# Optimization experiments

Hardware: AMD Instinct MI355X
Metric: run time of the kernel (lower is better)

The kernel has to match this reference:

```python
import jax, jax.numpy as jnp
import numpy as np

NUM_HEADS = 12
DIM = 768


def _ste_sign(x):
    # forward: sign with sign(0) = +1; backward: pass-through on |x| <= 1
    s = jnp.where(x >= 0, 1.0, -1.0).astype(x.dtype)
    base = jnp.clip(x, -1.0, 1.0)
    return base + jax.lax.stop_gradient(s - base)


def _quantize_qk(x):
    # s = mean(|x|) over last two dims (differentiable), times STE sign
    s = jnp.mean(jnp.abs(x), axis=(-2, -1), keepdims=True)
    return s * _ste_sign(x)


def _round_ste(z):
    return z + jax.lax.stop_gradient(jnp.round(z) - z)


def _quantize_p(x):
    qmax = 255.0
    s = 1.0 / qmax
    q = jnp.clip(_round_ste(x / s), 0.0, qmax)
    return s * q


def _quantize_v(x):
    # SymQuantizer fwd: per-column (dim=-2) absmax, detached; 8-bit symmetric
    m = jax.lax.stop_gradient(jnp.max(jnp.abs(x), axis=-2, keepdims=True))
    s = 127.0 / (m + 1e-6)
    qz = jnp.round(x * s) / (s + 1e-6)
    # backward STE: pass-through where -2 < x < 2 (clip_val = [-2, 2])
    base = jnp.clip(x, -2.0, 2.0)
    return base + jax.lax.stop_gradient(qz - base)


def _attention(x, w_qkv, w_proj, b_proj):
    B, C, H, W = x.shape
    N = H * W
    nh = NUM_HEADS
    hd = C // nh
    scale = hd ** (-0.5)
    xf = x.reshape(B, C, N).transpose(0, 2, 1)          # [B, N, C]
    qkv = xf @ w_qkv.T                                   # [B, N, 3C]
    qkv = qkv.reshape(B, N, 3, nh, hd).transpose(2, 0, 3, 1, 4)  # [3, B, h, N, d]
    q, k, v = qkv[0], qkv[1], qkv[2]
    q = _quantize_qk(q)
    k = _quantize_qk(k)
    attn = jnp.einsum('bhnd,bhmd->bhnm', q, k) * scale   # [B, h, N, N]
    attn = jax.nn.softmax(attn, axis=-1)
    attn = _quantize_p(attn)
    v = _quantize_v(v)
    out = jnp.einsum('bhnm,bhmd->bhnd', attn, v)         # [B, h, N, d]
    out = out.transpose(0, 2, 1, 3).reshape(B, N, C)
    out = out @ w_proj.T + b_proj                        # [B, N, C]
    return out.transpose(0, 2, 1).reshape(B, C, H, W)


def setup_inputs() -> dict:
    key = jax.random.key(0)
    k1, k2, k3, k4 = jax.random.split(key, 4)
    B, C, H, W = 16, DIM, 24, 24
    x = jax.random.normal(k1, (B, C, H, W), dtype=jnp.float32)
    w_qkv = jax.random.normal(k2, (3 * C, C), dtype=jnp.float32) * 0.02
    w_proj = jax.random.normal(k3, (C, C), dtype=jnp.float32) * 0.02
    b_proj = jax.random.normal(k4, (C,), dtype=jnp.float32) * 0.02
    return {"x": x, "w_qkv": w_qkv, "w_proj": w_proj, "b_proj": b_proj}


def reference(x, w_qkv, w_proj, b_proj):
    return _attention(x, w_qkv, w_proj, b_proj)
```

## Files before the change

### kernel.cpp

```cpp
#include <hip/hip_runtime.h>
#include <hip/hip_bf16.h>

#define B_   16
#define NH   12
#define NTOK 576
#define HD   64
#define CH   768
#define NELEM (B_*NH*NTOK*HD)
#define VT8SZ (NTOK*HD)
#define FIXCAP 16384
#define VPAD 176

typedef short v8s __attribute__((ext_vector_type(8)));
typedef short v4s __attribute__((ext_vector_type(4)));
typedef float v4f __attribute__((ext_vector_type(4)));
typedef int   v4i __attribute__((ext_vector_type(4)));

static __device__ __forceinline__ void split4(const float* f, v4s& hi, v4s& lo)
{
    #pragma unroll
    for (int i = 0; i < 4; ++i) {
        __hip_bfloat16 h = __float2bfloat16(f[i]);
        float hf = __bfloat162float(h);
        __hip_bfloat16 l = __float2bfloat16(f[i] - hf);
        hi[i] = __builtin_bit_cast(short, h);
        lo[i] = __builtin_bit_cast(short, l);
    }
}

__global__ __launch_bounds__(256) void qkv_mfma(const float* __restrict__ x,
    const float* __restrict__ w, float* __restrict__ q, float* __restrict__ k,
    float* __restrict__ v, int* __restrict__ fixn_g)
{
    if (blockIdx.x == 0 && threadIdx.x == 0) *fixn_g = 0;

    __shared__ short Ah[64*40], Al[64*40];
    __shared__ short Bh[256*40], Bl[256*40];
    const int tid = threadIdx.x;
    int g = blockIdx.x;
    g = (g & 7) * 162 + (g >> 3);
    const int b  = g / 81;
    const int rr = g % 81;
    const int jb = rr / 9;
    const int mb = rr % 9;
    const int n0 = mb * 64;
    const int j0 = jb * 256;
    const int lane = tid & 63, wv = tid >> 6;

    const int cq  = tid & 7;
    const int rw0 = tid >> 3;

    const float* xb  = x + (size_t)b * CH * NTOK + n0;
    const float* wbp = w + (size_t)j0 * CH;

    float areg[2][4];
    float breg[8][4];

    #pragma unroll
    for (int s = 0; s < 2; ++s) {
        const int nl = rw0 + 32*s;
        #pragma unroll
        for (int i = 0; i < 4; ++i)
            areg[s][i] = xb[(size_t)(cq*4 + i) * NTOK + nl];
    }
    #pragma unroll
    for (int s = 0; s < 8; ++s) {
        const int jl = rw0 + 32*s;
        const float4 t = *(const float4*)(wbp + (size_t)jl * CH + cq*4);
        breg[s][0]=t.x; breg[s][1]=t.y; breg[s][2]=t.z; breg[s][3]=t.w;
    }

    v4f acc[4][4];
    #pragma unroll
    for (int a = 0; a < 4; ++a)
        #pragma unroll
        for (int c = 0; c < 4; ++c) acc[a][c] = (v4f){0.f,0.f,0.f,0.f};

    for (int it = 0; it < 24; ++it) {
        __syncthreads();
        #pragma unroll
        for (int s = 0; s < 2; ++s) {
            v4s hi, lo; split4(areg[s], hi, lo);
            const int nl = rw0 + 32*s;
            *(v4s*)&Ah[nl*40 + cq*4] = hi;
            *(v4s*)&Al[nl*40 + cq*4] = lo;
        }
        #pragma unroll
        for (int s = 0; s < 8; ++s) {
            v4s hi, lo; split4(breg[s], hi, lo);
            const int jl = rw0 + 32*s;
            *(v4s*)&Bh[jl*40 + cq*4] = hi;
            *(v4s*)&Bl[jl*40 + cq*4] = lo;
        }
        __syncthreads();
        if (it < 23) {
            const int c0 = (it + 1) * 32;
            #pragma unroll
            for (int s = 0; s < 2; ++s) {
                const int nl = rw0 + 32*s;
                #pragma unroll
                for (int i = 0; i < 4; ++i)
                    areg[s][i] = xb[(size_t)(c0 + cq*4 + i) * NTOK + nl];
            }
            #pragma unroll
            for (int s = 0; s < 8; ++s) {
                const int jl = rw0 + 32*s;
                const float4 t = *(const float4*)(wbp + (size_t)jl * CH + c0 + cq*4);
                breg[s][0]=t.x; breg[s][1]=t.y; breg[s][2]=t.z; breg[s][3]=t.w;
            }
        }
        const int krow = lane & 15;
        const int k0   = (lane >> 4) * 8;
        v8s ah[4], al2[4], bh[4], bl[4];
        #pragma unroll
        for (int mt = 0; mt < 4; ++mt) {
            ah[mt]  = *(v8s*)&Ah[(mt*16 + krow)*40 + k0];
            al2[mt] = *(v8s*)&Al[(mt*16 + krow)*40 + k0];
        }
        #pragma unroll
        for (int jt = 0; jt < 4; ++jt) {
            bh[jt] = *(v8s*)&Bh[(wv*64 + jt*16 + krow)*40 + k0];
            bl[jt] = *(v8s*)&Bl[(wv*64 + jt*16 + krow)*40 + k0];
        }
        #pragma unroll
        for (int mt = 0; mt < 4; ++mt)
            #pragma unroll
            for (int jt = 0; jt < 4; ++jt) {
                acc[mt][jt] = __builtin_amdgcn_mfma_f32_16x16x32_bf16(ah[mt],  bh[jt], acc[mt][jt], 0, 0, 0);
                acc[mt][jt] = __builtin_amdgcn_mfma_f32_16x16x32_bf16(ah[mt],  bl[jt], acc[mt][jt], 0, 0, 0);
                acc[mt][jt] = __builtin_amdgcn_mfma_f32_16x16x32_bf16(al2[mt], bh[jt], acc[mt][jt], 0, 0, 0);
            }
    }

    const int sec = jb / 3;
    float* dst = (sec == 0) ? q : (sec == 1) ? k : v;
    const int h    = (jb % 3) * 4 + wv;
    const int col  = lane & 15;
    const int row4 = (lane >> 4) * 4;
    #pragma unroll
    for (int mt = 0; mt < 4; ++mt)
        #pragma unroll
        for (int jt = 0; jt < 4; ++jt) {
            const int dd = jt*16 + col;
            float* o = dst + (((size_t)b*NH + h)*NTOK + n0 + mt*16 + row4) * HD + dd;
            #pragma unroll
            for (int rg = 0; rg < 4; ++rg)
                o[(size_t)rg * HD] = acc[mt][jt][rg];
        }
}

__global__ __launch_bounds__(256) void reduce_pass(
    const float* __restrict__ q, const float* __restrict__ k,
    const float* __restrict__ v,
    unsigned long long* __restrict__ qm, unsigned long long* __restrict__ km,
    float* __restrict__ sumq_p, float* __restrict__ sumk_p,
    float* __restrict__ vmax_p, int* __restrict__ fixq_g,
    int* __restrict__ fixn_g)
{
    const int bh = blockIdx.x, ch = blockIdx.y;
    const int tid = threadIdx.x, lane = tid & 63, wv = tid >> 6;
    const size_t base = (size_t)bh * (NTOK * HD);
    const float* qb = q + base;
    const float* kb = k + base;
    const float* vb = v + base;
    const int n0 = ch * 144;

    float sq = 0.f, sk = 0.f, vmx = 0.f;
    for (int n = n0 + wv; n < n0 + 144; n += 4) {
        const float qv = qb[n*HD + lane];
        const float kv = kb[n*HD + lane];
        const float vv = vb[n*HD + lane];
        sq += fabsf(qv); sk += fabsf(kv); vmx = fmaxf(vmx, fabsf(vv));
        const unsigned long long mq = __ballot(qv >= 0.f);
        const unsigned long long mk = __ballot(kv >= 0.f);
        if (lane == 0) {
            qm[(size_t)bh*NTOK + n] = mq;
            km[(size_t)bh*NTOK + n] = mk;
        }
        if (fabsf(qv) < 1e-4f) {
            int s_ = atomicAdd(fixn_g, 1);
            if (s_ < FIXCAP) fixq_g[s_] = bh | (n << 8) | (lane << 18);
        }
        if (fabsf(kv) < 1e-4f) {
            int s_ = atomicAdd(fixn_g, 1);
            if (s_ < FIXCAP) fixq_g[s_] = bh | (n << 8) | (lane << 18) | (1 << 24);
        }
    }

    __shared__ float r1[256], r2[256], vm[256];
    r1[tid] = sq; r2[tid] = sk; vm[tid] = vmx;
    __syncthreads();
    for (int s = 128; s > 0; s >>= 1) {
        if (tid < s) { r1[tid] += r1[tid + s]; r2[tid] += r2[tid + s]; }
        __syncthreads();
    }
    if (tid == 0) { sumq_p[bh*4 + ch] = r1[0]; sumk_p[bh*4 + ch] = r2[0]; }
    if (tid < 64)
        vmax_p[((size_t)bh*4 + ch)*64 + tid] =
            fmaxf(fmaxf(vm[tid], vm[tid+64]), fmaxf(vm[tid+128], vm[tid+192]));
}

__global__ __launch_bounds__(64) void finalize(
    const float* __restrict__ sumq_p, const float* __restrict__ sumk_p,
    const float* __restrict__ vmax_p, float* __restrict__ cs,
    float* __restrict__ svs_g, float* __restrict__ scale_g)
{
    const int bh = blockIdx.x, d = threadIdx.x;
    if (d == 0) {
        const float msq = (sumq_p[bh*4] + sumq_p[bh*4+1] + sumq_p[bh*4+2] +
                           sumq_p[bh*4+3]) * (1.f / (NTOK * HD));
        const float msk = (sumk_p[bh*4] + sumk_p[bh*4+1] + sumk_p[bh*4+2] +
                           sumk_p[bh*4+3]) * (1.f / (NTOK * HD));
        cs[bh] = msq * msk * 0.125f;
    }
    const float mm = fmaxf(
        fmaxf(vmax_p[((size_t)bh*4+0)*64 + d], vmax_p[((size_t)bh*4+1)*64 + d]),
        fmaxf(vmax_p[((size_t)bh*4+2)*64 + d], vmax_p[((size_t)bh*4+3)*64 + d]));
    const float svs = 127.f / (mm + 1e-6f);
    svs_g[bh*64 + d] = svs;
    scale_g[bh*64 + d] = (1.f/255.f) / (svs + 1e-6f);
}

__global__ __launch_bounds__(256) void vquant(const float* __restrict__ v,
    const float* __restrict__ svs_g, unsigned char* __restrict__ vt8,
    int* __restrict__ csum_p)
{
    const int bh = blockIdx.x, ch = blockIdx.y;
    const int tid = threadIdx.x, d = tid & 63;
    const float* vb = v + (size_t)bh * NTOK * HD + ch * 144 * HD;
    __shared__ unsigned char vt[64 * VPAD];
    __shared__ int cs_l[256];
    const float s = svs_g[bh*64 + d];
    int part = 0;
    for (int i = tid; i < 144 * 64; i += 256) {
        const int nl = i >> 6;
        const int iq = (int)rintf(vb[i] * s);
        part += iq;
        vt[d*VPAD + nl] = (unsigned char)(iq & 255);
    }
    cs_l[tid] = part;
    __syncthreads();
    if (tid < 64)
        csum_p[((size_t)bh*4 + ch)*64 + tid] =
            cs_l[tid] + cs_l[tid+64] + cs_l[tid+128] + cs_l[tid+192];
    unsigned char* dst = vt8 + (size_t)bh * VT8SZ + ch * 144;
    for (int idx = tid; idx < 576; idx += 256) {
        const int row = idx / 9, seg = idx % 9;
        *(int4*)(dst + row*576 + seg*16) = *(const int4*)&vt[row*VPAD + seg*16];
    }
}

__global__ __launch_bounds__(256) void fixup(const float* __restrict__ x,
    const float* __restrict__ wqkv, unsigned long long* __restrict__ qm,
    unsigned long long* __restrict__ km, const int* __restrict__ fixq_g,
    const int* __restrict__ fixn_g)
{
    __shared__ float xls[4][CH];
    __shared__ float wls[4][CH];
    const int tid = threadIdx.x, lane = tid & 63, wv = tid >> 6;
    const int gw = blockIdx.x * 4 + wv;
    const int total = min(*fixn_g, FIXCAP);

    for (int e = gw; e < total; e += 256) {
        const int rec = fixq_g[e];
        const int bh  = rec & 255;
        const int n   = (rec >> 8) & 1023;
        const int dd  = (rec >> 18) & 63;
        const int isk = (rec >> 24) & 1;
        const int b = bh / NH, h = bh % NH;
        const float* wr = wqkv + (size_t)(isk*CH + h*HD + dd) * CH;
        const float* xr = x + (size_t)b * CH * NTOK + n;
        #pragma unroll
        for (int i = 0; i < 12; ++i) {
            const int c = i*64 + lane;
            xls[wv][c] = xr[(size_t)c * NTOK];
            wls[wv][c] = wr[c];
        }
        asm volatile("s_waitcnt vmcnt(0) lgkmcnt(0)" ::: "memory");
        float s = 0.f;
        #pragma unroll 8
        for (int c = 0; c < CH; ++c)
            s = fmaf(xls[wv][c], wls[wv][c], s);
        if (lane == 0) {
            unsigned* a32 = (unsigned*)((isk ? km : qm) + (size_t)bh*NTOK + n);
            const unsigned bit = 1u << (dd & 31);
            if (s >= 0.f) atomicOr(&a32[dd >> 5], bit);
            else          atomicAnd(&a32[dd >> 5], ~bit);
        }
        asm volatile("" ::: "memory");
    }
}

__global__ __launch_bounds__(256) void attn_i8(
    const unsigned long long* __restrict__ qm,
    const unsigned long long* __restrict__ km,
    const unsigned char* __restrict__ vt8, const float* __restrict__ cs,
    const int* __restrict__ csum_p, const float* __restrict__ scale_g,
    float* __restrict__ pre)
{
    const int tid = threadIdx.x;
    const int t0 = blockIdx.x << 6;
    const int h  = blockIdx.y;
    const int b  = blockIdx.z;
    const int bh = b * NH + h;

    __shared__ unsigned long long kml[NTOK];
    __shared__ unsigned long long qml[64];
    __shared__ float rs[64];
    __shared__ float table[65];
    __shared__ unsigned char vt[64*592];

    for (int i = tid; i < NTOK; i += 256) kml[i] = km[(size_t)bh * NTOK + i];
    if (tid < 64) qml[tid] = qm[(size_t)bh * NTOK + t0 + tid];
    const float c = cs[bh];
    if (tid < 65) table[tid] = __expf(c * (float)(64 - 2 * tid));
    {
        const unsigned char* src = vt8 + (size_t)bh * VT8SZ;
        #pragma unroll
        for (int t = 0; t < 9; ++t) {
            const int idx = tid + t*256;
            const int row = idx / 36, seg = idx % 36;
            *(int4*)&vt[row*592 + seg*16] = *(const int4*)(src + row*576 + seg*16);
        }
    }
    __syncthreads();

    const int wv = tid >> 6, lane = tid & 63;
    for (int r = wv; r < 64; r += 4) {
        const unsigned long long qq = qml[r];
        float s = 0.f;
        for (int m = lane; m < NTOK; m += 64) {
            const int pc = __popcll(qq ^ kml[m]);
            s += table[pc];
        }
        #pragma unroll
        for (int off = 32; off; off >>= 1) s += __shfl_xor(s, off, 64);
        if (lane == 0) rs[r] = 1.f / s;
    }
    __syncthreads();

    const int row_l = lane & 15;
    const int kgrp  = lane >> 4;
    const unsigned long long uq = qml[wv*16 + row_l];
    const float rsr = rs[wv*16 + row_l];
    v4i acc[4];
    #pragma unroll
    for (int jt = 0; jt < 4; ++jt) acc[jt] = (v4i){0,0,0,0};

    for (int ch = 0; ch < 9; ++ch) {
        const int mb = ch*64 + kgrp*16;
        int wds[4];
        #pragma unroll
        for (int wq = 0; wq < 4; ++wq) {
            int pk = 0;
            #pragma unroll
            for (int j = 0; j < 4; ++j) {
                const int pc = __popcll(uq ^ kml[mb + wq*4 + j]);
                const float p = table[pc] * rsr;
                const int iq = (int)rintf(p * 255.f) - 128;
                pk |= (iq & 255) << (8*j);
            }
            wds[wq] = pk;
        }
        v4i a; a[0]=wds[0]; a[1]=wds[1]; a[2]=wds[2]; a[3]=wds[3];
        #pragma unroll
        for (int jt = 0; jt < 4; ++jt) {
            const v4i bfr = *(const v4i*)&vt[(jt*16 + row_l)*592 + mb];
            acc[jt] = __builtin_amdgcn_mfma_i32_16x16x64_i8(a, bfr, acc[jt], 0, 0, 0);
        }
    }

    const int rb = kgrp * 4;
    #pragma unroll
    for (int jt = 0; jt < 4; ++jt) {
        const int dd = jt*16 + row_l;
        const int csd = csum_p[((size_t)bh*4+0)*64 + dd] +
                        csum_p[((size_t)bh*4+1)*64 + dd] +
                        csum_p[((size_t)bh*4+2)*64 + dd] +
                        csum_p[((size_t)bh*4+3)*64 + dd];
        const float scd = scale_g[bh*64 + dd];
        #pragma unroll
        for (int rg = 0; rg < 4; ++rg) {
            const int n = t0 + wv*16 + rb + rg;
            pre[((size_t)b * NTOK + n) * CH + h * HD + dd] =
                (float)(acc[jt][rg] + 128 * csd) * scd;
        }
    }
}

__global__ __launch_bounds__(256) void proj_mfma(const float* __restrict__ pre,
    const float* __restrict__ w, const float* __restrict__ bias,
    float* __restrict__ out)
{
    __shared__ short Awh[256*40], Awl[256*40];
    __shared__ short Bph[64*40],  Bpl[64*40];
    const int tid = threadIdx.x;
    int g = blockIdx.x;
    g = (g & 7) * 54 + (g >> 3);
    const int b  = g / 27;
    const int rr = g % 27;
    const int cb = rr / 9;
    const int nb = rr % 9;
    const int co0 = cb * 256;
    const int nn0 = nb * 64;
    const int lane = tid & 63, wv = tid >> 6;
    const int cq  = tid & 7;
    const int rw0 = tid >> 3;

    const float* wp = w + (size_t)co0 * CH;
    const float* pb = pre + ((size_t)b * NTOK + nn0) * CH;

    float areg[8][4];
    float breg[2][4];

    #pragma unroll
    for (int s = 0; s < 8; ++s) {
        const int cl = rw0 + 32*s;
        const float4 t = *(const float4*)(wp + (size_t)cl * CH + cq*4);
        areg[s][0]=t.x; areg[s][1]=t.y; areg[s][2]=t.z; areg[s][3]=t.w;
    }
    #pragma unroll
    for (int s = 0; s < 2; ++s) {
        const int nl = rw0 + 32*s;
        const float4 t = *(const float4*)(pb + (size_t)nl * CH + cq*4);
        breg[s][0]=t.x; breg[s][1]=t.y; breg[s][2]=t.z; breg[s][3]=t.w;
    }

    v4f acc[4][4];
    #pragma unroll
    for (int a = 0; a < 4; ++a)
        #pragma unroll
        for (int c = 0; c < 4; ++c) acc[a][c] = (v4f){0.f,0.f,0.f,0.f};

    for (int it = 0; it < 24; ++it) {
        __syncthreads();
        #pragma unroll
        for (int s = 0; s < 8; ++s) {
            v4s hi, lo; split4(areg[s], hi, lo);
            const int cl = rw0 + 32*s;
            *(v4s*)&Awh[cl*40 + cq*4] = hi;
            *(v4s*)&Awl[cl*40 + cq*4] = lo;
        }
        #pragma unroll
        for (int s = 0; s < 2; ++s) {
            v4s hi, lo; split4(breg[s], hi, lo);
            const int nl = rw0 + 32*s;
            *(v4s*)&Bph[nl*40 + cq*4] = hi;
            *(v4s*)&Bpl[nl*40 + cq*4] = lo;
        }
        __syncthreads();
        if (it < 23) {
            const int k0g = (it + 1) * 32;
            #pragma unroll
            for (int s = 0; s < 8; ++s) {
                const int cl = rw0 + 32*s;
                const float4 t = *(const float4*)(wp + (size_t)cl * CH + k0g + cq*4);
                areg[s][0]=t.x; areg[s][1]=t.y; areg[s][2]=t.z; areg[s][3]=t.w;
            }
            #pragma unroll
            for (int s = 0; s < 2; ++s) {
                const int nl = rw0 + 32*s;
                const float4 t = *(const float4*)(pb + (size_t)nl * CH + k0g + cq*4);
                breg[s][0]=t.x; breg[s][1]=t.y; breg[s][2]=t.z; breg[s][3]=t.w;
            }
        }
        const int krow = lane & 15;
        const int k0   = (lane >> 4) * 8;
        v8s ah[4], al2[4], bh[4], bl[4];
        #pragma unroll
        for (int mt = 0; mt < 4; ++mt) {
            ah[mt]  = *(v8s*)&Awh[(wv*64 + mt*16 + krow)*40 + k0];
            al2[mt] = *(v8s*)&Awl[(wv*64 + mt*16 + krow)*40 + k0];
        }
        #pragma unroll
        for (int jt = 0; jt < 4; ++jt) {
            bh[jt] = *(v8s*)&Bph[(jt*16 + krow)*40 + k0];
            bl[jt] = *(v8s*)&Bpl[(jt*16 + krow)*40 + k0];
        }
        #pragma unroll
        for (int mt = 0; mt < 4; ++mt)
            #pragma unroll
            for (int jt = 0; jt < 4; ++jt) {
                acc[mt][jt] = __builtin_amdgcn_mfma_f32_16x16x32_bf16(ah[mt],  bh[jt], acc[mt][jt], 0, 0, 0);
                acc[mt][jt] = __builtin_amdgcn_mfma_f32_16x16x32_bf16(ah[mt],  bl[jt], acc[mt][jt], 0, 0, 0);
                acc[mt][jt] = __builtin_amdgcn_mfma_f32_16x16x32_bf16(al2[mt], bh[jt], acc[mt][jt], 0, 0, 0);
            }
    }

    const int col  = lane & 15;
    const int row4 = (lane >> 4) * 4;
    #pragma unroll
    for (int mt = 0; mt < 4; ++mt)
        #pragma unroll
        for (int rg = 0; rg < 4; ++rg) {
            const int co = co0 + wv*64 + mt*16 + row4 + rg;
            const float bi = bias[co];
            #pragma unroll
            for (int jt = 0; jt < 4; ++jt)
                out[((size_t)b * CH + co) * NTOK + nn0 + jt*16 + col] =
                    acc[mt][jt][rg] + bi;
        }
}

extern "C" void kernel_launch(void* const* d_in, const int* in_sizes, int n_in,
                              void* d_out, int out_size, void* d_ws, size_t ws_size,
                              hipStream_t stream)
{
    (void)in_sizes; (void)n_in; (void)out_size; (void)ws_size;
    const float* x     = (const float*)d_in[0];
    const float* wqkv  = (const float*)d_in[1];
    const float* wproj = (const float*)d_in[2];
    const float* bproj = (const float*)d_in[3];
    float* out = (float*)d_out;

    float* qbuf = (float*)d_ws;
    float* kbuf = qbuf + NELEM;
    float* vbuf = kbuf + NELEM;
    unsigned long long* qmask = (unsigned long long*)(vbuf + NELEM);
    unsigned long long* kmask = qmask + (B_ * NH * NTOK);
    float* cs     = (float*)(kmask + (B_ * NH * NTOK));
    int*   csum_p = (int*)(cs + B_ * NH);
    float* scale  = (float*)(csum_p + B_ * NH * 4 * HD);
    float* svs_g  = scale + B_ * NH * HD;
    float* sumq_p = svs_g + B_ * NH * HD;
    float* sumk_p = sumq_p + B_ * NH * 4;
    float* vmax_p = sumk_p + B_ * NH * 4;
    int*   fixq_g = (int*)(vmax_p + B_ * NH * 4 * HD);
    int*   fixn_g = fixq_g + FIXCAP;
    unsigned char* vt8 = (unsigned char*)kbuf;

    qkv_mfma<<<dim3(1296), 256, 0, stream>>>(x, wqkv, qbuf, kbuf, vbuf, fixn_g);
    reduce_pass<<<dim3(B_*NH, 4), 256, 0, stream>>>(qbuf, kbuf, vbuf,
        qmask, kmask, sumq_p, sumk_p, vmax_p, fixq_g, fixn_g);
    finalize<<<dim3(B_*NH), 64, 0, stream>>>(sumq_p, sumk_p, vmax_p,
        cs, svs_g, scale);
    vquant<<<dim3(B_*NH, 4), 256, 0, stream>>>(vbuf, svs_g, vt8, csum_p);
    fixup<<<dim3(64), 256, 0, stream>>>(x, wqkv, qmask, kmask, fixq_g, fixn_g);
    attn_i8<<<dim3(9, NH, B_), 256, 0, stream>>>(qmask, kmask, vt8, cs,
                                                 csum_p, scale, qbuf);
    proj_mfma<<<dim3(432), 256, 0, stream>>>(qbuf, wproj, bproj, out);
}
```

Measured before the change: 454.9 us.

## Pre-split inputs to bf16 hi/lo and fuse Q/K reductions into QKV GEMM epilogue

Adds kernels that convert x (transposed to token-major) and both weight matrices into bf16 hi/lo pairs once, so the two GEMMs load ready-made bf16 tiles instead of splitting fp32 in their inner loops. The QKV GEMM epilogue now computes the Q/K sign masks, abs-sum partials, near-zero fixup list and V column max directly from accumulators. This removes the separate reduce pass and the fp32 Q/K writes and reads. The attention kernel writes its output pre-split for the projection. The cost is extra launches and splitting the weights on every call, plus more epilogue work with atomics in the GEMM.

```diff
diff --git a/kernel.cpp b/kernel.cpp
--- a/kernel.cpp
+++ b/kernel.cpp
@@ -16,24 +16,67 @@
 typedef float v4f __attribute__((ext_vector_type(4)));
 typedef int   v4i __attribute__((ext_vector_type(4)));
 
-static __device__ __forceinline__ void split4(const float* f, v4s& hi, v4s& lo)
-{
-    #pragma unroll
-    for (int i = 0; i < 4; ++i) {
-        __hip_bfloat16 h = __float2bfloat16(f[i]);
-        float hf = __bfloat162float(h);
-        __hip_bfloat16 l = __float2bfloat16(f[i] - hf);
-        hi[i] = __builtin_bit_cast(short, h);
-        lo[i] = __builtin_bit_cast(short, l);
-    }
-}
-
-__global__ __launch_bounds__(256) void qkv_mfma(const float* __restrict__ x,
-    const float* __restrict__ w, float* __restrict__ q, float* __restrict__ k,
-    float* __restrict__ v, int* __restrict__ fixn_g)
-{
-    if (blockIdx.x == 0 && threadIdx.x == 0) *fixn_g = 0;
-
+static __device__ __forceinline__ void split1(float f, short& h, short& l)
+{
+    __hip_bfloat16 bh = __float2bfloat16(f);
+    float hf = __bfloat162float(bh);
+    __hip_bfloat16 bl = __float2bfloat16(f - hf);
+    h = __builtin_bit_cast(short, bh);
+    l = __builtin_bit_cast(short, bl);
+}
+
+__global__ __launch_bounds__(256) void splitx(const float* __restrict__ x,
+    short* __restrict__ xh, short* __restrict__ xl, int* __restrict__ fixn_g)
+{
+    if (blockIdx.x == 0 && blockIdx.y == 0 && blockIdx.z == 0 &&
+        threadIdx.x == 0) *fixn_g = 0;
+    __shared__ float t[64][65];
+    const int n0 = blockIdx.x * 64, c0 = blockIdx.y * 64, b = blockIdx.z;
+    const int tid = threadIdx.x;
+    const int r4 = tid >> 6, cc = tid & 63;
+    #pragma unroll
+    for (int i = 0; i < 16; ++i) {
+        const int cl = r4 + i*4;
+        t[cl][cc] = x[((size_t)b*CH + c0 + cl)*NTOK + n0 + cc];
+    }
+    __syncthreads();
+    #pragma unroll
+    for (int i = 0; i < 16; ++i) {
+        const int nl = r4 + i*4;
+        short h, l; split1(t[cc][nl], h, l);
+        const size_t o = ((size_t)b*NTOK + n0 + nl)*CH + c0 + cc;
+        xh[o] = h; xl[o] = l;
+    }
+}
+
+__global__ __launch_bounds__(256) void splitw(const float* __restrict__ wq,
+    const float* __restrict__ wp, short* __restrict__ wqh,
+    short* __restrict__ wql, short* __restrict__ wph, short* __restrict__ wpl)
+{
+    const size_t e0 = (size_t)blockIdx.x * 4096 + threadIdx.x;
+    #pragma unroll
+    for (int i = 0; i < 16; ++i) {
+        const size_t e = e0 + (size_t)i * 256;
+        short h, l;
+        if (e < (size_t)2304*768) {
+            split1(wq[e], h, l);
+            wqh[e] = h; wql[e] = l;
+        } else {
+            const size_t o = e - (size_t)2304*768;
+            split1(wp[o], h, l);
+            wph[o] = h; wpl[o] = l;
+        }
+    }
+}
+
+__global__ __launch_bounds__(256) void qkv_mfma(const short* __restrict__ xh,
+    const short* __restrict__ xl, const short* __restrict__ wh,
+    const short* __restrict__ wl, float* __restrict__ v,
+    unsigned long long* __restrict__ qm, unsigned long long* __restrict__ km,
+    float* __restrict__ sumq_p, float* __restrict__ sumk_p,
+    float* __restrict__ vmax_p, int* __restrict__ fixq_g,
+    int* __restrict__ fixn_g)
+{
     __shared__ short Ah[64*40], Al[64*40];
     __shared__ short Bh[256*40], Bl[256*40];
     const int tid = threadIdx.x;
@@ -46,28 +89,26 @@
     const int n0 = mb * 64;
     const int j0 = jb * 256;
     const int lane = tid & 63, wv = tid >> 6;
-
     const int cq  = tid & 7;
     const int rw0 = tid >> 3;
 
-    const float* xb  = x + (size_t)b * CH * NTOK + n0;
-    const float* wbp = w + (size_t)j0 * CH;
-
-    float areg[2][4];
-    float breg[8][4];
-
+    const short* xbh = xh + ((size_t)b*NTOK + n0)*CH;
+    const short* xbl = xl + ((size_t)b*NTOK + n0)*CH;
+    const short* wbh = wh + (size_t)j0*CH;
+    const short* wbl = wl + (size_t)j0*CH;
+
+    v4s Ahr[2], Alr[2], Bhr[8], Blr[8];
     #pragma unroll
     for (int s = 0; s < 2; ++s) {
-        const int nl = rw0 + 32*s;
-        #pragma unroll
-        for (int i = 0; i < 4; ++i)
-            areg[s][i] = xb[(size_t)(cq*4 + i) * NTOK + nl];
+        const size_t o = (size_t)(rw0 + 32*s)*CH + cq*4;
+        Ahr[s] = *(const v4s*)&xbh[o];
+        Alr[s] = *(const v4s*)&xbl[o];
     }
     #pragma unroll
     for (int s = 0; s < 8; ++s) {
-        const int jl = rw0 + 32*s;
-        const float4 t = *(const float4*)(wbp + (size_t)jl * CH + cq*4);
-        breg[s][0]=t.x; breg[s][1]=t.y; breg[s][2]=t.z; breg[s][3]=t.w;
+        const size_t o = (size_t)(rw0 + 32*s)*CH + cq*4;
+        Bhr[s] = *(const v4s*)&wbh[o];
+        Blr[s] = *(const v4s*)&wbl[o];
     }
 
     v4f acc[4][4];
@@ -80,33 +121,30 @@
         __syncthreads();
         #pragma unroll
         for (int s = 0; s < 2; ++s) {
-            v4s hi, lo; split4(areg[s], hi, lo);
             const int nl = rw0 + 32*s;
-            *(v4s*)&Ah[nl*40 + cq*4] = hi;
-            *(v4s*)&Al[nl*40 + cq*4] = lo;
+            *(v4s*)&Ah[nl*40 + cq*4] = Ahr[s];
+            *(v4s*)&Al[nl*40 + cq*4] = Alr[s];
         }
         #pragma unroll
         for (int s = 0; s < 8; ++s) {
-            v4s hi, lo; split4(breg[s], hi, lo);
             const int jl = rw0 + 32*s;
-            *(v4s*)&Bh[jl*40 + cq*4] = hi;
-            *(v4s*)&Bl[jl*40 + cq*4] = lo;
+            *(v4s*)&Bh[jl*40 + cq*4] = Bhr[s];
+            *(v4s*)&Bl[jl*40 + cq*4] = Blr[s];
         }
         __syncthreads();
         if (it < 23) {
             const int c0 = (it + 1) * 32;
             #pragma unroll
             for (int s = 0; s < 2; ++s) {
-                const int nl = rw0 + 32*s;
-                #pragma unroll
-                for (int i = 0; i < 4; ++i)
-                    areg[s][i] = xb[(size_t)(c0 + cq*4 + i) * NTOK + nl];
+                const size_t o = (size_t)(rw0 + 32*s)*CH + c0 + cq*4;
+                Ahr[s] = *(const v4s*)&xbh[o];
+                Alr[s] = *(const v4s*)&xbl[o];
             }
             #pragma unroll
             for (int s = 0; s < 8; ++s) {
-                const int jl = rw0 + 32*s;
-                const float4 t = *(const float4*)(wbp + (size_t)jl * CH + c0 + cq*4);
-                breg[s][0]=t.x; breg[s][1]=t.y; breg[s][2]=t.z; breg[s][3]=t.w;
+                const size_t o = (size_t)(rw0 + 32*s)*CH + c0 + cq*4;
+                Bhr[s] = *(const v4s*)&wbh[o];
+                Blr[s] = *(const v4s*)&wbl[o];
             }
         }
         const int krow = lane & 15;
@@ -133,71 +171,83 @@
     }
 
     const int sec = jb / 3;
-    float* dst = (sec == 0) ? q : (sec == 1) ? k : v;
-    const int h    = (jb % 3) * 4 + wv;
-    const int col  = lane & 15;
-    const int row4 = (lane >> 4) * 4;
-    #pragma unroll
-    for (int mt = 0; mt < 4; ++mt)
+    const int h   = (jb % 3) * 4 + wv;
+    const int bh  = b * NH + h;
+    const int col = lane & 15, g4 = lane >> 4;
+
+    if (sec < 2) {
+        unsigned long long* mask = sec ? km : qm;
+        float* sump = sec ? sumk_p : sumq_p;
+        float asum = 0.f;
+        #pragma unroll
+        for (int mt = 0; mt < 4; ++mt)
+            #pragma unroll
+            for (int jt = 0; jt < 4; ++jt)
+                #pragma unroll
+                for (int rg = 0; rg < 4; ++rg)
+                    asum += fabsf(acc[mt][jt][rg]);
+        #pragma unroll
+        for (int off = 32; off; off >>= 1) asum += __shfl_xor(asum, off, 64);
+        if (lane == 0) sump[bh*9 + mb] = asum;
+
+        #pragma unroll
+        for (int mt = 0; mt < 4; ++mt)
+            #pragma unroll
+            for (int rg = 0; rg < 4; ++rg) {
+                const unsigned long long b0 = __ballot(acc[mt][0][rg] >= 0.f);
+                const unsigned long long b1 = __ballot(acc[mt][1][rg] >= 0.f);
+                const unsigned long long b2 = __ballot(acc[mt][2][rg] >= 0.f);
+                const unsigned long long b3 = __ballot(acc[mt][3][rg] >= 0.f);
+                if (col == 0) {
+                    const int sh = g4 * 16;
+                    const unsigned long long m =
+                          ((b0 >> sh) & 0xFFFFull)
+                        | (((b1 >> sh) & 0xFFFFull) << 16)
+                        | (((b2 >> sh) & 0xFFFFull) << 32)
+                        | (((b3 >> sh) & 0xFFFFull) << 48);
+                    const int n = n0 + mt*16 + g4*4 + rg;
+                    mask[(size_t)bh*NTOK + n] = m;
+                }
+            }
+        #pragma unroll
+        for (int mt = 0; mt < 4; ++mt)
+            #pragma unroll
+            for (int jt = 0; jt < 4; ++jt)
+                #pragma unroll
+                for (int rg = 0; rg < 4; ++rg)
+                    if (fabsf(acc[mt][jt][rg]) < 1e-4f) {
+                        const int n  = n0 + mt*16 + g4*4 + rg;
+                        const int dd = jt*16 + col;
+                        int s_ = atomicAdd(fixn_g, 1);
+                        if (s_ < FIXCAP)
+                            fixq_g[s_] = bh | (n<<8) | (dd<<18) | (sec<<24);
+                    }
+    } else {
+        const int row4 = g4 * 4;
+        #pragma unroll
+        for (int mt = 0; mt < 4; ++mt)
+            #pragma unroll
+            for (int jt = 0; jt < 4; ++jt) {
+                const int dd = jt*16 + col;
+                float* o = v + (((size_t)bh)*NTOK + n0 + mt*16 + row4)*HD + dd;
+                #pragma unroll
+                for (int rg = 0; rg < 4; ++rg)
+                    o[(size_t)rg * HD] = acc[mt][jt][rg];
+            }
         #pragma unroll
         for (int jt = 0; jt < 4; ++jt) {
-            const int dd = jt*16 + col;
-            float* o = dst + (((size_t)b*NH + h)*NTOK + n0 + mt*16 + row4) * HD + dd;
-            #pragma unroll
-            for (int rg = 0; rg < 4; ++rg)
-                o[(size_t)rg * HD] = acc[mt][jt][rg];
-        }
-}
-
-__global__ __launch_bounds__(256) void reduce_pass(
-    const float* __restrict__ q, const float* __restrict__ k,
-    const float* __restrict__ v,
-    unsigned long long* __restrict__ qm, unsigned long long* __restrict__ km,
-    float* __restrict__ sumq_p, float* __restrict__ sumk_p,
-    float* __restrict__ vmax_p, int* __restrict__ fixq_g,
-    int* __restrict__ fixn_g)
-{
-    const int bh = blockIdx.x, ch = blockIdx.y;
-    const int tid = threadIdx.x, lane = tid & 63, wv = tid >> 6;
-    const size_t base = (size_t)bh * (NTOK * HD);
-    const float* qb = q + base;
-    const float* kb = k + base;
-    const float* vb = v + base;
-    const int n0 = ch * 144;
-
-    float sq = 0.f, sk = 0.f, vmx = 0.f;
-    for (int n = n0 + wv; n < n0 + 144; n += 4) {
-        const float qv = qb[n*HD + lane];
-        const float kv = kb[n*HD + lane];
-        const float vv = vb[n*HD + lane];
-        sq += fabsf(qv); sk += fabsf(kv); vmx = fmaxf(vmx, fabsf(vv));
-        const unsigned long long mq = __ballot(qv >= 0.f);
-        const unsigned long long mk = __ballot(kv >= 0.f);
-        if (lane == 0) {
-            qm[(size_t)bh*NTOK + n] = mq;
-            km[(size_t)bh*NTOK + n] = mk;
-        }
-        if (fabsf(qv) < 1e-4f) {
-            int s_ = atomicAdd(fixn_g, 1);
-            if (s_ < FIXCAP) fixq_g[s_] = bh | (n << 8) | (lane << 18);
-        }
-        if (fabsf(kv) < 1e-4f) {
-            int s_ = atomicAdd(fixn_g, 1);
-            if (s_ < FIXCAP) fixq_g[s_] = bh | (n << 8) | (lane << 18) | (1 << 24);
-        }
-    }
-
-    __shared__ float r1[256], r2[256], vm[256];
-    r1[tid] = sq; r2[tid] = sk; vm[tid] = vmx;
-    __syncthreads();
-    for (int s = 128; s > 0; s >>= 1) {
-        if (tid < s) { r1[tid] += r1[tid + s]; r2[tid] += r2[tid + s]; }
-        __syncthreads();
-    }
-    if (tid == 0) { sumq_p[bh*4 + ch] = r1[0]; sumk_p[bh*4 + ch] = r2[0]; }
-    if (tid < 64)
-        vmax_p[((size_t)bh*4 + ch)*64 + tid] =
-            fmaxf(fmaxf(vm[tid], vm[tid+64]), fmaxf(vm[tid+128], vm[tid+192]));
+            float m = 0.f;
+            #pragma unroll
+            for (int mt = 0; mt < 4; ++mt)
+                #pragma unroll
+                for (int rg = 0; rg < 4; ++rg)
+                    m = fmaxf(m, fabsf(acc[mt][jt][rg]));
+            m = fmaxf(m, __shfl_xor(m, 16, 64));
+            m = fmaxf(m, __shfl_xor(m, 32, 64));
+            if (g4 == 0)
+                vmax_p[((size_t)bh*9 + mb)*64 + jt*16 + col] = m;
+        }
+    }
 }
 
 __global__ __launch_bounds__(64) void finalize(
@@ -207,15 +257,15 @@
 {
     const int bh = blockIdx.x, d = threadIdx.x;
     if (d == 0) {
-        const float msq = (sumq_p[bh*4] + sumq_p[bh*4+1] + sumq_p[bh*4+2] +
-                           sumq_p[bh*4+3]) * (1.f / (NTOK * HD));
-        const float msk = (sumk_p[bh*4] + sumk_p[bh*4+1] + sumk_p[bh*4+2] +
-                           sumk_p[bh*4+3]) * (1.f / (NTOK * HD));
-        cs[bh] = msq * msk * 0.125f;
-    }
-    const float mm = fmaxf(
-        fmaxf(vmax_p[((size_t)bh*4+0)*64 + d], vmax_p[((size_t)bh*4+1)*64 + d]),
-        fmaxf(vmax_p[((size_t)bh*4+2)*64 + d], vmax_p[((size_t)bh*4+3)*64 + d]));
+        float sq = 0.f, sk = 0.f;
+        #pragma unroll
+        for (int i = 0; i < 9; ++i) { sq += sumq_p[bh*9+i]; sk += sumk_p[bh*9+i]; }
+        cs[bh] = (sq * (1.f/(NTOK*HD))) * (sk * (1.f/(NTOK*HD))) * 0.125f;
+    }
+    float mm = 0.f;
+    #pragma unroll
+    for (int i = 0; i < 9; ++i)
+        mm = fmaxf(mm, vmax_p[((size_t)bh*9 + i)*64 + d]);
     const float svs = 127.f / (mm + 1e-6f);
     svs_g[bh*64 + d] = svs;
     scale_g[bh*64 + d] = (1.f/255.f) / (svs + 1e-6f);
@@ -296,7 +346,7 @@
     const unsigned long long* __restrict__ km,
     const unsigned char* __restrict__ vt8, const float* __restrict__ cs,
     const int* __restrict__ csum_p, const float* __restrict__ scale_g,
-    float* __restrict__ pre)
+    short* __restrict__ preh, short* __restrict__ prel)
 {
     const int tid = threadIdx.x;
     const int t0 = blockIdx.x << 6;
@@ -382,14 +432,17 @@
         #pragma unroll
         for (int rg = 0; rg < 4; ++rg) {
             const int n = t0 + wv*16 + rb + rg;
-            pre[((size_t)b * NTOK + n) * CH + h * HD + dd] =
-                (float)(acc[jt][rg] + 128 * csd) * scd;
-        }
-    }
-}
-
-__global__ __launch_bounds__(256) void proj_mfma(const float* __restrict__ pre,
-    const float* __restrict__ w, const float* __restrict__ bias,
+            const float f = (float)(acc[jt][rg] + 128 * csd) * scd;
+            short hh, ll; split1(f, hh, ll);
+            const size_t idx = ((size_t)b * NTOK + n) * CH + h * HD + dd;
+            preh[idx] = hh; prel[idx] = ll;
+        }
+    }
+}
+
+__global__ __launch_bounds__(256) void proj_mfma(const short* __restrict__ ph,
+    const short* __restrict__ pl, const short* __restrict__ wh,
+    const short* __restrict__ wl, const float* __restrict__ bias,
     float* __restrict__ out)
 {
     __shared__ short Awh[256*40], Awl[256*40];
@@ -407,23 +460,23 @@
     const int cq  = tid & 7;
     const int rw0 = tid >> 3;
 
-    const float* wp = w + (size_t)co0 * CH;
-    const float* pb = pre + ((size_t)b * NTOK + nn0) * CH;
-
-    float areg[8][4];
-    float breg[2][4];
-
+    const short* wph2 = wh + (size_t)co0 * CH;
+    const short* wpl2 = wl + (size_t)co0 * CH;
+    const short* pbh  = ph + ((size_t)b * NTOK + nn0) * CH;
+    const short* pbl  = pl + ((size_t)b * NTOK + nn0) * CH;
+
+    v4s Ahr[8], Alr[8], Bhr[2], Blr[2];
     #pragma unroll
     for (int s = 0; s < 8; ++s) {
-        const int cl = rw0 + 32*s;
-        const float4 t = *(const float4*)(wp + (size_t)cl * CH + cq*4);
-        areg[s][0]=t.x; areg[s][1]=t.y; areg[s][2]=t.z; areg[s][3]=t.w;
+        const size_t o = (size_t)(rw0 + 32*s)*CH + cq*4;
+        Ahr[s] = *(const v4s*)&wph2[o];
+        Alr[s] = *(const v4s*)&wpl2[o];
     }
     #pragma unroll
     for (int s = 0; s < 2; ++s) {
-        const int nl = rw0 + 32*s;
-        const float4 t = *(const float4*)(pb + (size_t)nl * CH + cq*4);
-        breg[s][0]=t.x; breg[s][1]=t.y; breg[s][2]=t.z; breg[s][3]=t.w;
+        const size_t o = (size_t)(rw0 + 32*s)*CH + cq*4;
+        Bhr[s] = *(const v4s*)&pbh[o];
+        Blr[s] = *(const v4s*)&pbl[o];
     }
 
     v4f acc[4][4];
@@ -436,32 +489,30 @@
         __syncthreads();
         #pragma unroll
         for (int s = 0; s < 8; ++s) {
-            v4s hi, lo; split4(areg[s], hi, lo);
             const int cl = rw0 + 32*s;
-            *(v4s*)&Awh[cl*40 + cq*4] = hi;
-            *(v4s*)&Awl[cl*40 + cq*4] = lo;
+            *(v4s*)&Awh[cl*40 + cq*4] = Ahr[s];
+            *(v4s*)&Awl[cl*40 + cq*4] = Alr[s];
         }
         #pragma unroll
         for (int s = 0; s < 2; ++s) {
-            v4s hi, lo; split4(breg[s], hi, lo);
             const int nl = rw0 + 32*s;
-            *(v4s*)&Bph[nl*40 + cq*4] = hi;
-            *(v4s*)&Bpl[nl*40 + cq*4] = lo;
+            *(v4s*)&Bph[nl*40 + cq*4] = Bhr[s];
+            *(v4s*)&Bpl[nl*40 + cq*4] = Blr[s];
         }
         __syncthreads();
         if (it < 23) {
             const int k0g = (it + 1) * 32;
             #pragma unroll
             for (int s = 0; s < 8; ++s) {
-                const int cl = rw0 + 32*s;
-                const float4 t = *(const float4*)(wp + (size_t)cl * CH + k0g + cq*4);
-                areg[s][0]=t.x; areg[s][1]=t.y; areg[s][2]=t.z; areg[s][3]=t.w;
+                const size_t o = (size_t)(rw0 + 32*s)*CH + k0g + cq*4;
+                Ahr[s] = *(const v4s*)&wph2[o];
+                Alr[s] = *(const v4s*)&wpl2[o];
             }
             #pragma unroll
             for (int s = 0; s < 2; ++s) {
-                const int nl = rw0 + 32*s;
-                const float4 t = *(const float4*)(pb + (size_t)nl * CH + k0g + cq*4);
-                breg[s][0]=t.x; breg[s][1]=t.y; breg[s][2]=t.z; breg[s][3]=t.w;
+                const size_t o = (size_t)(rw0 + 32*s)*CH + k0g + cq*4;
+                Bhr[s] = *(const v4s*)&pbh[o];
+                Blr[s] = *(const v4s*)&pbl[o];
             }
         }
         const int krow = lane & 15;
@@ -513,30 +564,38 @@
     const float* bproj = (const float*)d_in[3];
     float* out = (float*)d_out;
 
-    float* qbuf = (float*)d_ws;
-    float* kbuf = qbuf + NELEM;
-    float* vbuf = kbuf + NELEM;
-    unsigned long long* qmask = (unsigned long long*)(vbuf + NELEM);
-    unsigned long long* kmask = qmask + (B_ * NH * NTOK);
-    float* cs     = (float*)(kmask + (B_ * NH * NTOK));
-    int*   csum_p = (int*)(cs + B_ * NH);
-    float* scale  = (float*)(csum_p + B_ * NH * 4 * HD);
-    float* svs_g  = scale + B_ * NH * HD;
-    float* sumq_p = svs_g + B_ * NH * HD;
-    float* sumk_p = sumq_p + B_ * NH * 4;
-    float* vmax_p = sumk_p + B_ * NH * 4;
-    int*   fixq_g = (int*)(vmax_p + B_ * NH * 4 * HD);
+    float* vbuf = (float*)d_ws;
+    short* xh   = (short*)(vbuf + NELEM);
+    short* xl   = xh + NELEM;
+    short* wqh  = xl + NELEM;
+    short* wql  = wqh + 2304*768;
+    short* wph  = wql + 2304*768;
+    short* wpl  = wph + 768*768;
+    unsigned char* vt8 = (unsigned char*)(wpl + 768*768);
+    unsigned long long* qmask =
+        (unsigned long long*)(vt8 + (size_t)B_*NH*VT8SZ);
+    unsigned long long* kmask = qmask + (B_*NH*NTOK);
+    float* cs     = (float*)(kmask + (B_*NH*NTOK));
+    int*   csum_p = (int*)(cs + B_*NH);
+    float* scale  = (float*)(csum_p + B_*NH*4*HD);
+    float* svs_g  = scale + B_*NH*HD;
+    float* sumq_p = svs_g + B_*NH*HD;
+    float* sumk_p = sumq_p + B_*NH*9;
+    float* vmax_p = sumk_p + B_*NH*9;
+    int*   fixq_g = (int*)(vmax_p + B_*NH*9*HD);
     int*   fixn_g = fixq_g + FIXCAP;
-    unsigned char* vt8 = (unsigned char*)kbuf;
-
-    qkv_mfma<<<dim3(1296), 256, 0, stream>>>(x, wqkv, qbuf, kbuf, vbuf, fixn_g);
-    reduce_pass<<<dim3(B_*NH, 4), 256, 0, stream>>>(qbuf, kbuf, vbuf,
+    short* preh = xh;
+    short* prel = xl;
+
+    splitx<<<dim3(9, 12, B_), 256, 0, stream>>>(x, xh, xl, fixn_g);
+    splitw<<<dim3(576), 256, 0, stream>>>(wqkv, wproj, wqh, wql, wph, wpl);
+    qkv_mfma<<<dim3(1296), 256, 0, stream>>>(xh, xl, wqh, wql, vbuf,
         qmask, kmask, sumq_p, sumk_p, vmax_p, fixq_g, fixn_g);
     finalize<<<dim3(B_*NH), 64, 0, stream>>>(sumq_p, sumk_p, vmax_p,
         cs, svs_g, scale);
     vquant<<<dim3(B_*NH, 4), 256, 0, stream>>>(vbuf, svs_g, vt8, csum_p);
     fixup<<<dim3(64), 256, 0, stream>>>(x, wqkv, qmask, kmask, fixq_g, fixn_g);
     attn_i8<<<dim3(9, NH, B_), 256, 0, stream>>>(qmask, kmask, vt8, cs,
-                                                 csum_p, scale, qbuf);
-    proj_mfma<<<dim3(432), 256, 0, stream>>>(qbuf, wproj, bproj, out);
-}
+                                                 csum_p, scale, preh, prel);
+    proj_mfma<<<dim3(432), 256, 0, stream>>>(preh, prel, wph, wpl, bproj, out);
+}
```

Result: faster. 442.8 us (-2.7%).
